# Optimization experiments

Measured on AMD Instinct MI355X. Metric: run time of the kernel, lower is better.

The kernel has to match this reference:

```python
import jax, jax.numpy as jnp
import numpy as np

N_EXPERTS = 9
MODEL_DIM = 256
NUM_HEADS = 4
N_TOKENS = 4096
LN_EPS = 1e-5


def setup_inputs() -> dict:
    key0 = jax.random.key(0)
    ks = jax.random.split(key0, 8)
    D, E = MODEL_DIM, N_EXPERTS
    x = jax.random.normal(ks[0], (N_TOKENS, D), dtype=jnp.float32)
    label = jax.random.randint(ks[1], (N_TOKENS,), 0, E, dtype=jnp.int64)
    s = 0.02
    Wq = jax.random.normal(ks[2], (E, D, D), dtype=jnp.float32) * s
    Wk = jax.random.normal(ks[3], (E, D, D), dtype=jnp.float32) * s
    Wv = jax.random.normal(ks[4], (E, D, D), dtype=jnp.float32) * s
    bq = jnp.zeros((E, D), dtype=jnp.float32)
    bk = jnp.zeros((E, D), dtype=jnp.float32)
    bv = jnp.zeros((E, D), dtype=jnp.float32)
    Wf = jax.random.normal(ks[5], (D, D), dtype=jnp.float32) * s
    bf = jnp.zeros((D,), dtype=jnp.float32)
    gamma = jnp.ones((D,), dtype=jnp.float32)
    beta = jnp.zeros((D,), dtype=jnp.float32)
    return {"x": x, "label": label, "Wq": Wq, "bq": bq, "Wk": Wk, "bk": bk,
            "Wv": Wv, "bv": bv, "Wf": Wf, "bf": bf, "gamma": gamma, "beta": beta}


def reference(x, label, Wq, bq, Wk, bk, Wv, bv, Wf, bf, gamma, beta):
    # v2 path: per-label expert QKV projection + within-label self-attention.
    N, D = x.shape
    H = NUM_HEADS
    dph = D // H  # dim_per_head = 64
    # NOTE: source uses scale = (dim_per_head // num_heads) ** -0.5
    scale = float((dph // H)) ** -0.5
    idx = jnp.arange(N)
    lbl = label.astype(jnp.int32)

    # Compute all 9 expert projections, then select per-token (dense dispatch).
    q = jnp.einsum('nd,edh->enh', x, Wq)[lbl, idx] + bq[lbl]  # [N, D]
    k = jnp.einsum('nd,edh->enh', x, Wk)[lbl, idx] + bk[lbl]
    v = jnp.einsum('nd,edh->enh', x, Wv)[lbl, idx] + bv[lbl]

    qh = q.reshape(N, H, dph)
    kh = k.reshape(N, H, dph)
    vh = v.reshape(N, H, dph)

    # Attention restricted to tokens with the same label (equivalent to the
    # per-label gather -> bmm -> scatter in the torch loop).
    scores = jnp.einsum('nhd,mhd->hnm', qh, kh) * scale  # [H, N, N]
    same = (lbl[:, None] == lbl[None, :])  # [N, N]
    scores = jnp.where(same[None, :, :], scores, -jnp.inf)
    attn = jax.nn.softmax(scores, axis=-1)
    ctx = jnp.einsum('hnm,mhd->nhd', attn, vh).reshape(N, D)

    out = ctx @ Wf + bf
    h = x + out  # residual is the (gathered) original key
    mean = jnp.mean(h, axis=-1, keepdims=True)
    var = jnp.mean(jnp.square(h - mean), axis=-1, keepdims=True)
    return gamma * (h - mean) / jnp.sqrt(var + LN_EPS) + beta
```

## Files before the change

### kernel.cpp

```cpp
#include <hip/hip_runtime.h>
#include <math.h>

#define N_TOK 4096
#define DIM 256
#define NHEAD 4
#define DPH 64
#define NEXP 9
#define SCALE 0.25f
#define MAXST 80
#define GPAD 4736
#define VPITCH 4736
#define NSPLIT 2

typedef short s8 __attribute__((ext_vector_type(8)));
typedef short s4 __attribute__((ext_vector_type(4)));
typedef float f4 __attribute__((ext_vector_type(4)));

static __device__ __forceinline__ short f2bf(float f) {
  union { float f; unsigned u; } v;
  v.f = f;
  unsigned r = (v.u + 0x7FFFu + ((v.u >> 16) & 1u)) >> 16;
  return (short)r;
}

static __device__ __forceinline__ float wave_sum(float v) {
#pragma unroll
  for (int o = 32; o > 0; o >>= 1) v += __shfl_xor(v, o, 64);
  return v;
}

__global__ __launch_bounds__(256) void k_prep(
    const float* __restrict__ x, const int* __restrict__ label,
    const float* __restrict__ Wq, const float* __restrict__ Wk,
    const float* __restrict__ Wv, const float* __restrict__ Wf,
    int* __restrict__ perm, int* __restrict__ iperm, int* __restrict__ gs,
    int* __restrict__ gep, int* __restrict__ st_e, int* __restrict__ st_row,
    int* __restrict__ nstp, short* __restrict__ WbT, short* __restrict__ xb) {
  int b = blockIdx.x;
  int tid = threadIdx.x;
  if (b == 0) {
    __shared__ int cntL[NEXP], baseL[NEXP];
    if (tid < NEXP) cntL[tid] = 0;
    __syncthreads();
    for (int t = tid; t < N_TOK; t += 256) atomicAdd(&cntL[label[t]], 1);
    __syncthreads();
    if (tid == 0) {
      int run = 0, ns = 0;
      for (int e = 0; e < NEXP; e++) {
        gs[e] = run;
        baseL[e] = run;
        int end = run + cntL[e];
        gep[e] = end;
        for (int r = run; r < end; r += 64) {
          st_e[ns] = e;
          st_row[ns] = r;
          ns++;
        }
        run = (end + 63) & ~63;
      }
      *nstp = ns;
    }
    __syncthreads();
    for (int t = tid; t < N_TOK; t += 256) {
      int pos = atomicAdd(&baseL[label[t]], 1);
      perm[pos] = t;
      iperm[t] = pos;
    }
  } else if (b <= 448) {
    __shared__ short tile[64 * 68];
    int vt = b - 1;
    int slab = vt >> 4;
    const float* src = (slab < 9)    ? Wq + (size_t)slab * 65536
                       : (slab < 18) ? Wk + (size_t)(slab - 9) * 65536
                       : (slab < 27) ? Wv + (size_t)(slab - 18) * 65536
                                     : Wf;
    int xy = vt & 15;
    int d0 = (xy >> 2) * 64, h0 = (xy & 3) * 64;
    int rl = tid >> 4;
    int hh = (tid & 15) * 4;
#pragma unroll
    for (int p = 0; p < 4; p++) {
      int dl = p * 16 + rl;
      float4 v = *(const float4*)(src + (size_t)(d0 + dl) * 256 + h0 + hh);
      s4 o;
      o[0] = f2bf(v.x); o[1] = f2bf(v.y); o[2] = f2bf(v.z); o[3] = f2bf(v.w);
      *(s4*)&tile[dl * 68 + hh] = o;
    }
    __syncthreads();
    int h = tid >> 2, dq = (tid & 3) * 16;
    s8 pa, pb;
#pragma unroll
    for (int i = 0; i < 8; i++) {
      pa[i] = tile[(dq + i) * 68 + h];
      pb[i] = tile[(dq + 8 + i) * 68 + h];
    }
    short* dst = WbT + (size_t)slab * 65536 + (size_t)(h0 + h) * 256 + d0 + dq;
    *(s8*)dst = pa;
    *(s8*)(dst + 8) = pb;
  } else {
    int tok = (b - 449) * 64 + (tid >> 2);
    int qd = (tid & 3) * 64;
    const float* src = x + (size_t)tok * DIM + qd;
    short* dst = xb + (size_t)tok * DIM + qd;
#pragma unroll
    for (int i = 0; i < 16; i++) {
      float4 v = *(const float4*)(src + i * 4);
      s4 o;
      o[0] = f2bf(v.x); o[1] = f2bf(v.y); o[2] = f2bf(v.z); o[3] = f2bf(v.w);
      *(s4*)(dst + i * 4) = o;
    }
  }
}

__global__ __launch_bounds__(256) void k_proj(
    const short* __restrict__ xb, const short* __restrict__ WbT,
    const float* __restrict__ bq, const float* __restrict__ bk,
    const float* __restrict__ bv, const int* __restrict__ perm,
    const int* __restrict__ gep, const int* __restrict__ st_e,
    const int* __restrict__ st_row, const int* __restrict__ nstp,
    short* __restrict__ qg, short* __restrict__ kg, short* __restrict__ vgT) {
  int b = blockIdx.x;
  if (b >= *nstp) return;
  int gy = blockIdx.y;
  int mtx = blockIdx.z;
  int e = st_e[b];
  int row0 = st_row[b];
  int g1 = gep[e];
  int tid = threadIdx.x, wl = tid >> 6, lane = tid & 63;
  int m = lane & 15, quad = lane >> 4;

  __shared__ short st_s[4][16 * 72];

  int row = row0 + wl * 16 + m;
  int pr = perm[(row < g1) ? row : row0];
  const short* Ap = xb + (size_t)pr * DIM + quad * 8;
  const short* Bp = WbT + (size_t)(mtx * 9 + e) * 65536 +
                    (size_t)(gy * 64 + m) * 256 + quad * 8;
  const float* bias = (mtx == 0) ? bq : (mtx == 1) ? bk : bv;

  s8 ac = *(const s8*)Ap;
  s8 bc[4];
#pragma unroll
  for (int t = 0; t < 4; t++) bc[t] = *(const s8*)(Bp + t * 16 * 256);
  f4 acc[4];
#pragma unroll
  for (int t = 0; t < 4; t++) acc[t] = (f4){0.f, 0.f, 0.f, 0.f};
#pragma unroll
  for (int kc = 0; kc < 8; kc++) {
    s8 an = ac;
    s8 bn[4] = {bc[0], bc[1], bc[2], bc[3]};
    if (kc < 7) {
      an = *(const s8*)(Ap + (kc + 1) * 32);
#pragma unroll
      for (int t = 0; t < 4; t++)
        bn[t] = *(const s8*)(Bp + t * 16 * 256 + (kc + 1) * 32);
    }
#pragma unroll
    for (int t = 0; t < 4; t++)
      acc[t] = __builtin_amdgcn_mfma_f32_16x16x32_bf16(ac, bc[t], acc[t], 0, 0, 0);
    ac = an;
#pragma unroll
    for (int t = 0; t < 4; t++) bc[t] = bn[t];
  }

  if (mtx == 2) {
#pragma unroll
    for (int t = 0; t < 4; t++) {
      int col = gy * 64 + t * 16 + m;
      float bs = bias[e * DIM + col];
      s4 o;
#pragma unroll
      for (int r = 0; r < 4; r++) o[r] = f2bf(acc[t][r] + bs);
      *(s4*)&vgT[(size_t)col * VPITCH + row0 + wl * 16 + quad * 4] = o;
    }
  } else {
    short* ws = st_s[wl];
#pragma unroll
    for (int t = 0; t < 4; t++) {
      int col = gy * 64 + t * 16 + m;
      float bs = bias[e * DIM + col];
#pragma unroll
      for (int r = 0; r < 4; r++)
        ws[(quad * 4 + r) * 72 + t * 16 + m] = f2bf(acc[t][r] + bs);
    }
    int rr = lane >> 2, cg2 = (lane & 3) * 16;
    s8 v0 = *(s8*)&ws[rr * 72 + cg2];
    s8 v1 = *(s8*)&ws[rr * 72 + cg2 + 8];
    short* dst = ((mtx == 1) ? kg : qg) +
                 (size_t)(row0 + wl * 16 + rr) * DIM + gy * 64 + cg2;
    *(s8*)dst = v0;
    *(s8*)(dst + 8) = v1;
  }
}

__global__ __launch_bounds__(256) void k_attn(
    const short* __restrict__ qg, const short* __restrict__ kg,
    const short* __restrict__ vgT, const int* __restrict__ gs,
    const int* __restrict__ gep, const int* __restrict__ st_e,
    const int* __restrict__ st_row, const int* __restrict__ nstp,
    float* __restrict__ Op, float* __restrict__ lp) {
  int b = blockIdx.x;
  if (b >= *nstp) return;
  int h = blockIdx.y;
  int sp = blockIdx.z;
  int e = st_e[b];
  int row0 = st_row[b];
  int g0 = gs[e], kend = gep[e];
  int ntiles = (kend - g0 + 63) >> 6;
  int tpc = (ntiles + NSPLIT - 1) / NSPLIT;
  int t0i = sp * tpc;
  int t1i = min(ntiles, t0i + tpc);
  int start = g0 + t0i * 64, end = g0 + t1i * 64;

  int tid = threadIdx.x;
  int wl = tid >> 6, lane = tid & 63;
  int m = lane & 15, quad = lane >> 4;
  int r0 = tid >> 3;
  int c0 = (tid & 7) * 8;

  __shared__ short k_s[64 * 72];
  __shared__ short v_s[64 * 72];
  __shared__ short p_s[4 * 16 * 72];

  f4 o_acc[4];
  float l_r[4];
#pragma unroll
  for (int t = 0; t < 4; t++) o_acc[t] = (f4){0.f, 0.f, 0.f, 0.f};
#pragma unroll
  for (int r = 0; r < 4; r++) l_r[r] = 0.f;

  if (start < end) {
    int qrow = row0 + wl * 16 + m;
    if (qrow >= kend) qrow = row0;
    s8 qf0 = *(const s8*)&qg[(size_t)qrow * DIM + h * DPH + quad * 8];
    s8 qf1 = *(const s8*)&qg[(size_t)qrow * DIM + h * DPH + 32 + quad * 8];

    s8 pk0, pk1, pv0, pv1;
#define PREF(JT)                                                              \
  do {                                                                        \
    pk0 = *(const s8*)&kg[(size_t)((JT) + r0) * DIM + h * DPH + c0];          \
    pk1 = *(const s8*)&kg[(size_t)((JT) + r0 + 32) * DIM + h * DPH + c0];     \
    pv0 = *(const s8*)&vgT[(size_t)(h * DPH + r0) * VPITCH + (JT) + c0];      \
    pv1 = *(const s8*)&vgT[(size_t)(h * DPH + r0 + 32) * VPITCH + (JT) + c0]; \
  } while (0)

    PREF(start);
    for (int jt = start; jt < end; jt += 64) {
      __syncthreads();
      *(s8*)&k_s[r0 * 72 + c0] = pk0;
      *(s8*)&k_s[(r0 + 32) * 72 + c0] = pk1;
      *(s8*)&v_s[r0 * 72 + c0] = pv0;
      *(s8*)&v_s[(r0 + 32) * 72 + c0] = pv1;
      int jn = jt + 64;
      if (jn < end) PREF(jn);
      __syncthreads();

      f4 s_acc[4];
#pragma unroll
      for (int t = 0; t < 4; t++) s_acc[t] = (f4){0.f, 0.f, 0.f, 0.f};
#pragma unroll
      for (int t = 0; t < 4; t++) {
        s8 kb0 = *(s8*)&k_s[(t * 16 + m) * 72 + quad * 8];
        s8 kb1 = *(s8*)&k_s[(t * 16 + m) * 72 + 32 + quad * 8];
        s_acc[t] = __builtin_amdgcn_mfma_f32_16x16x32_bf16(qf0, kb0, s_acc[t], 0, 0, 0);
        s_acc[t] = __builtin_amdgcn_mfma_f32_16x16x32_bf16(qf1, kb1, s_acc[t], 0, 0, 0);
      }

#pragma unroll
      for (int t = 0; t < 4; t++) {
        bool ok = (jt + t * 16 + m) < kend;
#pragma unroll
        for (int r = 0; r < 4; r++) {
          float p = ok ? __expf(s_acc[t][r] * SCALE) : 0.f;
          l_r[r] += p;
          p_s[(wl * 16 + quad * 4 + r) * 72 + t * 16 + m] = f2bf(p);
        }
      }

#pragma unroll
      for (int kk = 0; kk < 2; kk++) {
        s8 pa = *(s8*)&p_s[(wl * 16 + m) * 72 + kk * 32 + quad * 8];
#pragma unroll
        for (int t = 0; t < 4; t++) {
          s8 vb = *(s8*)&v_s[(t * 16 + m) * 72 + kk * 32 + quad * 8];
          o_acc[t] = __builtin_amdgcn_mfma_f32_16x16x32_bf16(pa, vb, o_acc[t], 0, 0, 0);
        }
      }
    }
#undef PREF
  }

  float* Ob = Op + (size_t)sp * GPAD * DIM;
#pragma unroll
  for (int r = 0; r < 4; r++) {
    float lt = l_r[r];
#pragma unroll
    for (int o = 8; o > 0; o >>= 1) lt += __shfl_xor(lt, o, 64);
    int grow = row0 + wl * 16 + quad * 4 + r;
    if (m == 0) lp[(size_t)(sp * NHEAD + h) * GPAD + grow] = lt;
#pragma unroll
    for (int t = 0; t < 4; t++)
      Ob[(size_t)grow * DIM + h * DPH + t * 16 + m] = o_acc[t][r];
  }
}

__global__ __launch_bounds__(256) void k_out(
    const float* __restrict__ Op, const float* __restrict__ lp,
    const int* __restrict__ iperm, const short* __restrict__ WbT,
    const float* __restrict__ x, const float* __restrict__ bfv,
    const float* __restrict__ gamma, const float* __restrict__ beta,
    float* __restrict__ out) {
  int t0 = blockIdx.x * 16;
  int tid = threadIdx.x, wl = tid >> 6, lane = tid & 63;
  int m = lane & 15, quad = lane >> 4;
  __shared__ float h_s[16 * 260];

  int grow = iperm[t0 + m];
  float inv[NHEAD];
#pragma unroll
  for (int h = 0; h < NHEAD; h++) {
    float s = 0.f;
#pragma unroll
    for (int sp = 0; sp < NSPLIT; sp++)
      s += lp[(size_t)(sp * NHEAD + h) * GPAD + grow];
    inv[h] = 1.f / s;
  }

  s8 af[8];
#pragma unroll
  for (int kc = 0; kc < 8; kc++) {
    f4 s0 = (f4){0.f, 0.f, 0.f, 0.f}, s1 = (f4){0.f, 0.f, 0.f, 0.f};
#pragma unroll
    for (int sp = 0; sp < NSPLIT; sp++) {
      const float* p =
          Op + ((size_t)sp * GPAD + grow) * DIM + kc * 32 + quad * 8;
      s0 += *(const f4*)p;
      s1 += *(const f4*)(p + 4);
    }
    float iv = inv[kc >> 1];
#pragma unroll
    for (int j = 0; j < 4; j++) {
      af[kc][j] = f2bf(s0[j] * iv);
      af[kc][4 + j] = f2bf(s1[j] * iv);
    }
  }

  const short* Bp =
      WbT + (size_t)27 * 65536 + (size_t)(wl * 64 + m) * 256 + quad * 8;
  f4 acc[4];
#pragma unroll
  for (int t = 0; t < 4; t++) acc[t] = (f4){0.f, 0.f, 0.f, 0.f};
#pragma unroll
  for (int kc = 0; kc < 8; kc++)
#pragma unroll
    for (int t = 0; t < 4; t++) {
      s8 wb = *(const s8*)(Bp + t * 16 * 256 + kc * 32);
      acc[t] = __builtin_amdgcn_mfma_f32_16x16x32_bf16(af[kc], wb, acc[t], 0, 0, 0);
    }

#pragma unroll
  for (int t = 0; t < 4; t++) {
    int col = wl * 64 + t * 16 + m;
    float bs = bfv[col];
#pragma unroll
    for (int r = 0; r < 4; r++) h_s[(quad * 4 + r) * 260 + col] = acc[t][r] + bs;
  }
  __syncthreads();

#pragma unroll
  for (int rr = 0; rr < 4; rr++) {
    int row = wl * 4 + rr;
    float hv[4];
#pragma unroll
    for (int k2 = 0; k2 < 4; k2++)
      hv[k2] = h_s[row * 260 + lane + 64 * k2] +
               x[(size_t)(t0 + row) * DIM + lane + 64 * k2];
    float mean = wave_sum(hv[0] + hv[1] + hv[2] + hv[3]) * (1.f / 256.f);
    float sq = 0.f;
#pragma unroll
    for (int k2 = 0; k2 < 4; k2++) {
      float dd = hv[k2] - mean;
      sq += dd * dd;
    }
    float rstd = rsqrtf(wave_sum(sq) * (1.f / 256.f) + 1e-5f);
#pragma unroll
    for (int k2 = 0; k2 < 4; k2++) {
      int c = lane + 64 * k2;
      out[(size_t)(t0 + row) * DIM + c] =
          gamma[c] * ((hv[k2] - mean) * rstd) + beta[c];
    }
  }
}

extern "C" void kernel_launch(void* const* d_in, const int* in_sizes, int n_in,
                              void* d_out, int out_size, void* d_ws,
                              size_t ws_size, hipStream_t stream) {
  const float* x = (const float*)d_in[0];
  const int* label = (const int*)d_in[1];
  const float* Wq = (const float*)d_in[2];
  const float* bq = (const float*)d_in[3];
  const float* Wk = (const float*)d_in[4];
  const float* bk = (const float*)d_in[5];
  const float* Wv = (const float*)d_in[6];
  const float* bv = (const float*)d_in[7];
  const float* Wf = (const float*)d_in[8];
  const float* bfv = (const float*)d_in[9];
  const float* gamma = (const float*)d_in[10];
  const float* beta = (const float*)d_in[11];
  float* out = (float*)d_out;

  int* perm = (int*)d_ws;
  int* iperm = perm + 4800;
  int* gs = iperm + 4096;
  int* gep = gs + 16;
  int* st_e = gep + 16;
  int* st_row = st_e + 128;
  int* nstp = st_row + 128;
  short* qg = (short*)((char*)d_ws + 65536);
  short* kg = qg + (size_t)GPAD * DIM;
  short* vgT = kg + (size_t)GPAD * DIM;
  short* WbT = vgT + (size_t)DIM * VPITCH;
  short* xb = WbT + (size_t)28 * 65536;
  float* Op = (float*)(xb + (size_t)N_TOK * DIM);
  float* lp = Op + (size_t)NSPLIT * GPAD * DIM;

  hipLaunchKernelGGL(k_prep, dim3(513), dim3(256), 0, stream, x, label, Wq, Wk,
                     Wv, Wf, perm, iperm, gs, gep, st_e, st_row, nstp, WbT, xb);
  hipLaunchKernelGGL(k_proj, dim3(MAXST, 4, 3), dim3(256), 0, stream, xb, WbT,
                     bq, bk, bv, perm, gep, st_e, st_row, nstp, qg, kg, vgT);
  hipLaunchKernelGGL(k_attn, dim3(MAXST, NHEAD, NSPLIT), dim3(256), 0, stream,
                     qg, kg, vgT, gs, gep, st_e, st_row, nstp, Op, lp);
  hipLaunchKernelGGL(k_out, dim3(N_TOK / 16), dim3(256), 0, stream, Op, lp,
                     iperm, WbT, x, bfv, gamma, beta, out);
}
```

Measured before the change: 140.4 us.

## Double-buffer K/V LDS tiles in attention and use wave ballots for label binning

```diff
diff --git a/kernel.cpp b/kernel.cpp
--- a/kernel.cpp
+++ b/kernel.cpp
@@ -40,9 +40,21 @@
   int tid = threadIdx.x;
   if (b == 0) {
     __shared__ int cntL[NEXP], baseL[NEXP];
+    int wl = tid >> 6, lane = tid & 63;
     if (tid < NEXP) cntL[tid] = 0;
     __syncthreads();
-    for (int t = tid; t < N_TOK; t += 256) atomicAdd(&cntL[label[t]], 1);
+    int lab[16];
+#pragma unroll
+    for (int i = 0; i < 16; i++) lab[i] = label[(wl * 16 + i) * 64 + lane];
+#pragma unroll
+    for (int i = 0; i < 16; i++) {
+#pragma unroll
+      for (int e = 0; e < NEXP; e++) {
+        unsigned long long mk = __ballot(lab[i] == e);
+        int c = __popcll(mk);
+        if (c && lane == 0) atomicAdd(&cntL[e], c);
+      }
+    }
     __syncthreads();
     if (tid == 0) {
       int run = 0, ns = 0;
@@ -61,8 +73,23 @@
       *nstp = ns;
     }
     __syncthreads();
-    for (int t = tid; t < N_TOK; t += 256) {
-      int pos = atomicAdd(&baseL[label[t]], 1);
+#pragma unroll
+    for (int i = 0; i < 16; i++) {
+      int t = (wl * 16 + i) * 64 + lane;
+      int lv = lab[i];
+      int pos = 0;
+#pragma unroll
+      for (int e = 0; e < NEXP; e++) {
+        unsigned long long mk = __ballot(lv == e);
+        int c = __popcll(mk);
+        if (c) {
+          int src = __ffsll((unsigned long long)mk) - 1;
+          int base = 0;
+          if (lane == src) base = atomicAdd(&baseL[e], c);
+          base = __shfl(base, src, 64);
+          if (lv == e) pos = base + __popcll(mk & ((1ull << lane) - 1ull));
+        }
+      }
       perm[pos] = t;
       iperm[t] = pos;
     }
@@ -218,8 +245,8 @@
   int r0 = tid >> 3;
   int c0 = (tid & 7) * 8;
 
-  __shared__ short k_s[64 * 72];
-  __shared__ short v_s[64 * 72];
+  __shared__ short k_s[2][64 * 72];
+  __shared__ short v_s[2][64 * 72];
   __shared__ short p_s[4 * 16 * 72];
 
   f4 o_acc[4];
@@ -243,25 +270,30 @@
     pv0 = *(const s8*)&vgT[(size_t)(h * DPH + r0) * VPITCH + (JT) + c0];      \
     pv1 = *(const s8*)&vgT[(size_t)(h * DPH + r0 + 32) * VPITCH + (JT) + c0]; \
   } while (0)
+#define STORE(SL)                            \
+  do {                                       \
+    *(s8*)&k_s[SL][r0 * 72 + c0] = pk0;      \
+    *(s8*)&k_s[SL][(r0 + 32) * 72 + c0] = pk1; \
+    *(s8*)&v_s[SL][r0 * 72 + c0] = pv0;      \
+    *(s8*)&v_s[SL][(r0 + 32) * 72 + c0] = pv1; \
+  } while (0)
 
     PREF(start);
+    STORE(0);
+    int cur = 0;
     for (int jt = start; jt < end; jt += 64) {
+      int jn = jt + 64;
+      bool havenext = jn < end;
+      if (havenext) PREF(jn);
       __syncthreads();
-      *(s8*)&k_s[r0 * 72 + c0] = pk0;
-      *(s8*)&k_s[(r0 + 32) * 72 + c0] = pk1;
-      *(s8*)&v_s[r0 * 72 + c0] = pv0;
-      *(s8*)&v_s[(r0 + 32) * 72 + c0] = pv1;
-      int jn = jt + 64;
-      if (jn < end) PREF(jn);
-      __syncthreads();
 
       f4 s_acc[4];
 #pragma unroll
       for (int t = 0; t < 4; t++) s_acc[t] = (f4){0.f, 0.f, 0.f, 0.f};
 #pragma unroll
       for (int t = 0; t < 4; t++) {
-        s8 kb0 = *(s8*)&k_s[(t * 16 + m) * 72 + quad * 8];
-        s8 kb1 = *(s8*)&k_s[(t * 16 + m) * 72 + 32 + quad * 8];
+        s8 kb0 = *(s8*)&k_s[cur][(t * 16 + m) * 72 + quad * 8];
+        s8 kb1 = *(s8*)&k_s[cur][(t * 16 + m) * 72 + 32 + quad * 8];
         s_acc[t] = __builtin_amdgcn_mfma_f32_16x16x32_bf16(qf0, kb0, s_acc[t], 0, 0, 0);
         s_acc[t] = __builtin_amdgcn_mfma_f32_16x16x32_bf16(qf1, kb1, s_acc[t], 0, 0, 0);
       }
@@ -282,12 +314,16 @@
         s8 pa = *(s8*)&p_s[(wl * 16 + m) * 72 + kk * 32 + quad * 8];
 #pragma unroll
         for (int t = 0; t < 4; t++) {
-          s8 vb = *(s8*)&v_s[(t * 16 + m) * 72 + kk * 32 + quad * 8];
+          s8 vb = *(s8*)&v_s[cur][(t * 16 + m) * 72 + kk * 32 + quad * 8];
           o_acc[t] = __builtin_amdgcn_mfma_f32_16x16x32_bf16(pa, vb, o_acc[t], 0, 0, 0);
         }
       }
+
+      if (havenext) STORE(cur ^ 1);
+      cur ^= 1;
     }
 #undef PREF
+#undef STORE
   }
 
   float* Ob = Op + (size_t)sp * GPAD * DIM;
```

Measured after the change: 164.8 us. 17.3% more time.
